# Performance work log

Measured on AMD Instinct MI355X. Metric: run time of the kernel, lower is better.

## Reference

```python
import jax, jax.numpy as jnp
import numpy as np
from jax import lax


def _conv2d(x, w, b, stride):
    # x: [B,C,H,W], w: [O,I,kh,kw], b: [O]
    y = lax.conv_general_dilated(
        x, w, window_strides=(stride, stride), padding='VALID',
        dimension_numbers=('NCHW', 'OIHW', 'NCHW'))
    return y + b[None, :, None, None]


def setup_inputs() -> dict:
    key = jax.random.key(0)
    ks = jax.random.split(key, 4)
    B, C, H, W = 8, 128, 128, 128
    x = jax.random.normal(ks[0], (B, C, H, W), dtype=jnp.float32)
    # conv weights, scaled like torch default init (~1/sqrt(fan_in))
    Wq = jax.random.normal(ks[1], (C, C, 2, 2), dtype=jnp.float32) / np.sqrt(C * 4)
    Wk = jax.random.normal(ks[2], (C, C, 2, 2), dtype=jnp.float32) / np.sqrt(C * 4)
    Wv = jax.random.normal(ks[3], (C, C, 1, 1), dtype=jnp.float32) / np.sqrt(C)
    bq = jnp.zeros((C,), dtype=jnp.float32)
    bk = jnp.zeros((C,), dtype=jnp.float32)
    bv = jnp.zeros((C,), dtype=jnp.float32)
    return {'x': x, 'Wq': Wq, 'bq': bq, 'Wk': Wk, 'bk': bk, 'Wv': Wv, 'bv': bv}


def reference(x, Wq, bq, Wk, bk, Wv, bv):
    B, C, H, W = x.shape
    # query/key: 2x2 stride-2 convs -> [B, C, (H//2)*(W//2)]
    q = _conv2d(x, Wq, bq, 2).reshape(B, C, -1)
    k = _conv2d(x, Wk, bk, 2).reshape(B, C, -1)
    # value: 1x1 conv -> [B, C, H*W]
    v = _conv2d(x, Wv, bv, 1).reshape(B, C, -1)
    # energy: [B, C, C]
    energy = jnp.einsum('bcn,bdn->bcd', q, k)
    # max-subtract trick: softmax over (row_max - energy)
    energy_new = jnp.max(energy, axis=-1, keepdims=True) - energy
    attention = jax.nn.softmax(energy_new, axis=-1)
    out = jnp.einsum('bcd,bdn->bcn', attention, v)
    return out.reshape(B, C, H, W)
```

## Files before the change

### kernel.cpp

```cpp
#include <hip/hip_runtime.h>
#include <math.h>


typedef float f32x4 __attribute__((ext_vector_type(4)));
typedef short s16x8 __attribute__((ext_vector_type(8)));

__device__ __forceinline__ unsigned short f2bf(float f) {
  union { float f; unsigned u; } v; v.f = f;
  unsigned r = v.u + 0x7FFFu + ((v.u >> 16) & 1u);
  return (unsigned short)(r >> 16);
}
__device__ __forceinline__ float bf2f(unsigned short h) {
  union { unsigned u; float f; } v; v.u = ((unsigned)h) << 16;
  return v.f;
}
__device__ __forceinline__ unsigned pack2(unsigned short a, unsigned short b) {
  return (unsigned)a | ((unsigned)b << 16);
}

__global__ __launch_bounds__(256) void k_prep(
    const float* __restrict__ Wq, const float* __restrict__ Wk,
    unsigned short* __restrict__ Wth, unsigned short* __restrict__ Wtl) {
  const int f = (blockIdx.x * 256 + threadIdx.x) * 4;
  const int row = f >> 9;
  const int k   = f & 511;
  const float* src = (row < 128) ? &Wq[row * 512 + k] : &Wk[(row - 128) * 512 + k];
  float4 v = *(const float4*)src;
  unsigned short h0 = f2bf(v.x), h1 = f2bf(v.y), h2 = f2bf(v.z), h3 = f2bf(v.w);
  unsigned short l0 = f2bf(v.x - bf2f(h0)), l1 = f2bf(v.y - bf2f(h1));
  unsigned short l2 = f2bf(v.z - bf2f(h2)), l3 = f2bf(v.w - bf2f(h3));
  const int di = (k >> 5) * 8192 + row * 32 + (k & 31);
  *(ushort4*)&Wth[di] = make_ushort4(h0, h1, h2, h3);
  *(ushort4*)&Wtl[di] = make_ushort4(l0, l1, l2, l3);
}

__global__ __launch_bounds__(256, 2) void k_conv_energy(
    const float* __restrict__ x,
    const unsigned short* __restrict__ Wth, const unsigned short* __restrict__ Wtl,
    const float* __restrict__ bq, const float* __restrict__ bk,
    float* __restrict__ epart) {
  __shared__ unsigned short LDS[32768];
  unsigned short* Th = LDS;
  unsigned short* Tl = LDS + 16384;

  const int t = threadIdx.x;
  const int nt = blockIdx.x, b = blockIdx.y;
  const int w = t >> 6, lane = t & 63;
  const int lrow = lane & 15, lkb = lane >> 4;

  const int pp = t >> 4;
  const int ci_l = pp >> 1, kh = pp & 1;
  const int i16 = t & 15;
  const int klb = ci_l * 4 + kh * 2;
  const float* xb = x + ((size_t)b << 21);
  const float* xrow = xb + (size_t)ci_l * 16384 + (2 * nt + kh) * 128 + 2 * i16;

  f32x4 acc[4][4];
#pragma unroll
  for (int m = 0; m < 4; ++m)
#pragma unroll
    for (int n = 0; n < 4; ++n) acc[m][n] = (f32x4){0.f, 0.f, 0.f, 0.f};

  s16x8 pfh[2][4], pfl[2][4];
  s16x8 bfh[2][4], bfl[2][4];
  float2 pv[2][4];
  const int aoff = (w * 64 + lrow) * 32 + lkb * 8;

#pragma unroll
  for (int m = 0; m < 4; ++m) {
    pfh[0][m] = *(const s16x8*)&Wth[aoff + m * 512];
    pfl[0][m] = *(const s16x8*)&Wtl[aoff + m * 512];
    pfh[1][m] = *(const s16x8*)&Wth[8192 + aoff + m * 512];
    pfl[1][m] = *(const s16x8*)&Wtl[8192 + aoff + m * 512];
  }
#pragma unroll
  for (int g = 0; g < 4; ++g) pv[1][g] = *(const float2*)&xrow[32 * g];
  {
    unsigned short* Nh = LDS;
    unsigned short* Nl = LDS + 2560;
#pragma unroll
    for (int g = 0; g < 4; ++g) {
      const int n = i16 + 16 * g;
      unsigned short hx = f2bf(pv[1][g].x), hy = f2bf(pv[1][g].y);
      *(unsigned*)&Nh[n * 40 + klb] = pack2(hx, hy);
      *(unsigned*)&Nl[n * 40 + klb] = pack2(f2bf(pv[1][g].x - bf2f(hx)),
                                            f2bf(pv[1][g].y - bf2f(hy)));
    }
  }
#pragma unroll
  for (int g = 0; g < 4; ++g)
    pv[1][g] = *(const float2*)&xrow[(size_t)8 * 16384 + 32 * g];
  __syncthreads();
#pragma unroll
  for (int nf = 0; nf < 4; ++nf) {
    const int bidx = (nf * 16 + lrow) * 40 + lkb * 8;
    bfh[0][nf] = *(const s16x8*)&LDS[bidx];
    bfl[0][nf] = *(const s16x8*)&LDS[2560 + bidx];
  }

#pragma unroll
  for (int step = 0; step < 16; ++step) {
    const int cur = step & 1;
    if (step < 15) {
      unsigned short* Nh = LDS + (cur ^ 1) * 5120;
      unsigned short* Nl = Nh + 2560;
#pragma unroll
      for (int g = 0; g < 4; ++g) {
        const int n = i16 + 16 * g;
        unsigned short hx = f2bf(pv[cur ^ 1][g].x), hy = f2bf(pv[cur ^ 1][g].y);
        *(unsigned*)&Nh[n * 40 + klb] = pack2(hx, hy);
        *(unsigned*)&Nl[n * 40 + klb] = pack2(f2bf(pv[cur ^ 1][g].x - bf2f(hx)),
                                              f2bf(pv[cur ^ 1][g].y - bf2f(hy)));
      }
    }
    __syncthreads();
    if (step < 15) {
      const unsigned short* Bh = LDS + (cur ^ 1) * 5120;
      const unsigned short* Bl = Bh + 2560;
#pragma unroll
      for (int nf = 0; nf < 4; ++nf) {
        const int bidx = (nf * 16 + lrow) * 40 + lkb * 8;
        bfh[cur ^ 1][nf] = *(const s16x8*)&Bh[bidx];
        bfl[cur ^ 1][nf] = *(const s16x8*)&Bl[bidx];
      }
    }
    if (step < 14) {
#pragma unroll
      for (int g = 0; g < 4; ++g)
        pv[cur][g] = *(const float2*)&xrow[(size_t)(step + 2) * 8 * 16384 + 32 * g];
    }
#pragma unroll
    for (int m = 0; m < 4; ++m)
#pragma unroll
      for (int n = 0; n < 4; ++n) {
        acc[m][n] = __builtin_amdgcn_mfma_f32_16x16x32_bf16(pfh[cur][m], bfh[cur][n], acc[m][n], 0, 0, 0);
        acc[m][n] = __builtin_amdgcn_mfma_f32_16x16x32_bf16(pfh[cur][m], bfl[cur][n], acc[m][n], 0, 0, 0);
        acc[m][n] = __builtin_amdgcn_mfma_f32_16x16x32_bf16(pfl[cur][m], bfh[cur][n], acc[m][n], 0, 0, 0);
      }
    if (step < 14) {
      const unsigned short* Wh_n = Wth + (step + 2) * 8192;
      const unsigned short* Wl_n = Wtl + (step + 2) * 8192;
#pragma unroll
      for (int m = 0; m < 4; ++m) {
        pfh[cur][m] = *(const s16x8*)&Wh_n[aoff + m * 512];
        pfl[cur][m] = *(const s16x8*)&Wl_n[aoff + m * 512];
      }
    }
  }
  __syncthreads();

  const float* biasp = (w < 2) ? bq : bk;
  const int rb = (w & 1) * 64;
  float biasr[16];
#pragma unroll
  for (int m = 0; m < 4; ++m)
#pragma unroll
    for (int i = 0; i < 4; ++i)
      biasr[m * 4 + i] = biasp[rb + m * 16 + (lane >> 4) * 4 + i];

#pragma unroll
  for (int m = 0; m < 4; ++m) {
    const int r0 = w * 64 + m * 16 + (lane >> 4) * 4;
#pragma unroll
    for (int n = 0; n < 4; ++n) {
      const int c = n * 16 + lrow;
      const int c8 = c >> 3, c7 = c & 7;
#pragma unroll
      for (int i = 0; i < 4; ++i) {
        const int r = r0 + i;
        const float vv = acc[m][n][i] + biasr[m * 4 + i];
        const unsigned short h = f2bf(vv);
        const unsigned short l = f2bf(vv - bf2f(h));
        const int ad = r * 64 + (((c8 ^ (r & 7))) << 3) + c7;
        Th[ad] = h;
        Tl[ad] = l;
      }
    }
  }
  __syncthreads();

  f32x4 e[4][4];
#pragma unroll
  for (int m = 0; m < 4; ++m)
#pragma unroll
    for (int n = 0; n < 4; ++n) e[m][n] = (f32x4){0.f, 0.f, 0.f, 0.f};

  const int mrow0 = (w >> 1) * 64;
  const int nrow0 = 128 + (w & 1) * 64;
#pragma unroll
  for (int ks = 0; ks < 2; ++ks) {
    const int c8 = ks * 4 + lkb;
    s16x8 qh[4], ql[4], kh8[4], kl8[4];
#pragma unroll
    for (int m = 0; m < 4; ++m) {
      const int r = mrow0 + m * 16 + lrow;
      const int ad = r * 64 + ((c8 ^ (r & 7)) << 3);
      qh[m] = *(const s16x8*)&Th[ad];
      ql[m] = *(const s16x8*)&Tl[ad];
    }
#pragma unroll
    for (int n = 0; n < 4; ++n) {
      const int r = nrow0 + n * 16 + lrow;
      const int ad = r * 64 + ((c8 ^ (r & 7)) << 3);
      kh8[n] = *(const s16x8*)&Th[ad];
      kl8[n] = *(const s16x8*)&Tl[ad];
    }
#pragma unroll
    for (int m = 0; m < 4; ++m)
#pragma unroll
      for (int n = 0; n < 4; ++n) {
        e[m][n] = __builtin_amdgcn_mfma_f32_16x16x32_bf16(qh[m], kh8[n], e[m][n], 0, 0, 0);
        e[m][n] = __builtin_amdgcn_mfma_f32_16x16x32_bf16(qh[m], kl8[n], e[m][n], 0, 0, 0);
        e[m][n] = __builtin_amdgcn_mfma_f32_16x16x32_bf16(ql[m], kh8[n], e[m][n], 0, 0, 0);
      }
  }
  float* ep = epart + ((size_t)b * 64 + nt) * 16384;
#pragma unroll
  for (int m = 0; m < 4; ++m) {
    const int qr = (w >> 1) * 64 + m * 16 + (lane >> 4) * 4;
#pragma unroll
    for (int n = 0; n < 4; ++n) {
      const int kr = (w & 1) * 64 + n * 16 + lrow;
#pragma unroll
      for (int i = 0; i < 4; ++i) ep[(size_t)(qr + i) * 128 + kr] = e[m][n][i];
    }
  }
}

__global__ __launch_bounds__(256) void k_softmax_M(
    const float* __restrict__ epart, const float* __restrict__ Wv,
    const float* __restrict__ bv, float* __restrict__ Mbuf,
    float* __restrict__ outbb) {
  __shared__ float As[4][128];
  const int t = threadIdx.x;
  const int wid = t >> 6, lane = t & 63;
  const int b = blockIdx.x >> 5;
  const int c = (blockIdx.x & 31) * 4 + wid;
  const int d0 = lane * 2;

  float2 s = make_float2(0.f, 0.f);
#pragma unroll 4
  for (int p = 0; p < 64; ++p) {
    float2 e = *(const float2*)&epart[((size_t)b * 64 + p) * 16384 + c * 128 + d0];
    s.x += e.x; s.y += e.y;
  }
  float mn = fminf(s.x, s.y);
#pragma unroll
  for (int off = 1; off < 64; off <<= 1) mn = fminf(mn, __shfl_xor(mn, off));
  const float p0 = expf(mn - s.x);
  const float p1 = expf(mn - s.y);
  float tot = p0 + p1;
#pragma unroll
  for (int off = 1; off < 64; off <<= 1) tot += __shfl_xor(tot, off);
  const float inv = 1.f / tot;
  const float a0 = p0 * inv, a1 = p1 * inv;

  const float2 bvv = *(const float2*)&bv[d0];
  float ob = a0 * bvv.x + a1 * bvv.y;
#pragma unroll
  for (int off = 1; off < 64; off <<= 1) ob += __shfl_xor(ob, off);
  if (lane == 0) outbb[b * 128 + c] = ob;

  As[wid][d0] = a0;
  As[wid][d0 + 1] = a1;
  float m0 = 0.f, m1 = 0.f;
#pragma unroll 4
  for (int d = 0; d < 128; ++d) {
    const float a = As[wid][d];
    const float2 wv = *(const float2*)&Wv[d * 128 + d0];
    m0 = fmaf(a, wv.x, m0);
    m1 = fmaf(a, wv.y, m1);
  }
  *(float2*)&Mbuf[(size_t)b * 16384 + c * 128 + d0] = make_float2(m0, m1);
}

__global__ __launch_bounds__(256) void k_out(
    const float* __restrict__ x, const float* __restrict__ Mbuf,
    const float* __restrict__ outbb, float* __restrict__ out) {
  __shared__ unsigned short Ms[128 * 40];
  __shared__ unsigned short Xs[128 * 40];
  const int t = threadIdx.x;
  const int nt = blockIdx.x, b = blockIdx.y;
  const int wid = t >> 6, lane = t & 63;
  const int wr = wid >> 1, wc = wid & 1;
  const int lrow = lane & 15, lkb = lane >> 4;
  const int am = t >> 1, ak0 = (t & 1) * 16;
  const int xkl = (t >> 5) * 4;
  const int xc0 = (t & 31) * 4;

  const float* xb = x + ((size_t)b << 21);
  const float* Mb = Mbuf + (size_t)b * 16384;
  float* ob = out + ((size_t)b << 21);

  f32x4 acc[4][4];
#pragma unroll
  for (int m = 0; m < 4; ++m)
#pragma unroll
    for (int n = 0; n < 4; ++n) acc[m][n] = (f32x4){0.f, 0.f, 0.f, 0.f};

  for (int step = 0; step < 4; ++step) {
    const int kk = step * 32;
    {
      float w[16];
      *(float4*)&w[0]  = *(const float4*)&Mb[am * 128 + kk + ak0];
      *(float4*)&w[4]  = *(const float4*)&Mb[am * 128 + kk + ak0 + 4];
      *(float4*)&w[8]  = *(const float4*)&Mb[am * 128 + kk + ak0 + 8];
      *(float4*)&w[12] = *(const float4*)&Mb[am * 128 + kk + ak0 + 12];
      unsigned short hs[16];
#pragma unroll
      for (int i = 0; i < 16; ++i) hs[i] = f2bf(w[i]);
      *(uint4*)&Ms[am * 40 + ak0]     = *(uint4*)&hs[0];
      *(uint4*)&Ms[am * 40 + ak0 + 8] = *(uint4*)&hs[8];
    }
#pragma unroll
    for (int q = 0; q < 4; ++q) {
      const int kl = xkl + q;
      float4 v = *(const float4*)&xb[(size_t)(kk + kl) * 16384 + nt * 128 + xc0];
      Xs[(xc0 + 0) * 40 + kl] = f2bf(v.x);
      Xs[(xc0 + 1) * 40 + kl] = f2bf(v.y);
      Xs[(xc0 + 2) * 40 + kl] = f2bf(v.z);
      Xs[(xc0 + 3) * 40 + kl] = f2bf(v.w);
    }
    __syncthreads();
    s16x8 af[4], bf[4];
#pragma unroll
    for (int m = 0; m < 4; ++m)
      af[m] = *(const s16x8*)&Ms[(wr * 64 + m * 16 + lrow) * 40 + lkb * 8];
#pragma unroll
    for (int n = 0; n < 4; ++n)
      bf[n] = *(const s16x8*)&Xs[(wc * 64 + n * 16 + lrow) * 40 + lkb * 8];
#pragma unroll
    for (int m = 0; m < 4; ++m)
#pragma unroll
      for (int n = 0; n < 4; ++n)
        acc[m][n] = __builtin_amdgcn_mfma_f32_16x16x32_bf16(af[m], bf[n], acc[m][n], 0, 0, 0);
    __syncthreads();
  }
#pragma unroll
  for (int m = 0; m < 4; ++m) {
    const int r0 = wr * 64 + m * 16 + (lane >> 4) * 4;
#pragma unroll
    for (int n = 0; n < 4; ++n) {
      const int gc = nt * 128 + wc * 64 + n * 16 + (lane & 15);
#pragma unroll
      for (int i = 0; i < 4; ++i) {
        const int row = r0 + i;
        ob[(size_t)row * 16384 + gc] = acc[m][n][i] + outbb[b * 128 + row];
      }
    }
  }
}

extern "C" void kernel_launch(void* const* d_in, const int* in_sizes, int n_in,
                              void* d_out, int out_size, void* d_ws, size_t ws_size,
                              hipStream_t stream) {
  const float* x  = (const float*)d_in[0];
  const float* Wq = (const float*)d_in[1];
  const float* bq = (const float*)d_in[2];
  const float* Wk = (const float*)d_in[3];
  const float* bk = (const float*)d_in[4];
  const float* Wv = (const float*)d_in[5];
  const float* bv = (const float*)d_in[6];
  float* out = (float*)d_out;
  char* ws = (char*)d_ws;

  float* epart = (float*)ws;
  float* Mbuf  = (float*)(ws + 33554432);
  float* outbb = (float*)(ws + 34078720);
  unsigned short* Wth = (unsigned short*)(ws + 34082816);
  unsigned short* Wtl = (unsigned short*)(ws + 34344960);

  hipLaunchKernelGGL(k_prep, dim3(128), dim3(256), 0, stream, Wq, Wk, Wth, Wtl);
  hipLaunchKernelGGL(k_conv_energy, dim3(64, 8), dim3(256), 0, stream,
                     x, Wth, Wtl, bq, bk, epart);
  hipLaunchKernelGGL(k_softmax_M, dim3(256), dim3(256), 0, stream,
                     epart, Wv, bv, Mbuf, outbb);
  hipLaunchKernelGGL(k_out, dim3(128, 8), dim3(256), 0, stream,
                     x, Mbuf, outbb, out);
}
```

Before: 87.04 us.

## Enlarge conv-energy tile to 128 spatial columns with 512-thread blocks

The fused conv+energy kernel now uses 512-thread blocks, each covering two output rows (128 spatial positions) instead of one. Eight waves split the tile as 4x2 over output channels and spatial columns, so weight fragments are reused across twice the spatial width. This halves the number of per-block partial energy matrices written to and summed from the workspace. The main loop is reordered with a single raw barrier per step, the energy stage runs in four k-chunks with a smaller LDS buffer, and f2bf now uses the native __bf16 conversion. In exchange, fewer blocks are launched (256 instead of 512), registers per thread rise, and there are more barriers in the energy stage.

```diff
diff --git a/kernel.cpp b/kernel.cpp
--- a/kernel.cpp
+++ b/kernel.cpp
@@ -6,9 +6,9 @@
 typedef short s16x8 __attribute__((ext_vector_type(8)));
 
 __device__ __forceinline__ unsigned short f2bf(float f) {
-  union { float f; unsigned u; } v; v.f = f;
-  unsigned r = v.u + 0x7FFFu + ((v.u >> 16) & 1u);
-  return (unsigned short)(r >> 16);
+  union { __bf16 b; unsigned short u; } v;
+  v.b = (__bf16)f;
+  return v.u;
 }
 __device__ __forceinline__ float bf2f(unsigned short h) {
   union { unsigned u; float f; } v; v.u = ((unsigned)h) << 16;
@@ -34,26 +34,27 @@
   *(ushort4*)&Wtl[di] = make_ushort4(l0, l1, l2, l3);
 }
 
-__global__ __launch_bounds__(256, 2) void k_conv_energy(
+__global__ __launch_bounds__(512) void k_conv_energy(
     const float* __restrict__ x,
     const unsigned short* __restrict__ Wth, const unsigned short* __restrict__ Wtl,
     const float* __restrict__ bq, const float* __restrict__ bk,
     float* __restrict__ epart) {
-  __shared__ unsigned short LDS[32768];
+  __shared__ unsigned short LDS[20480];
   unsigned short* Th = LDS;
-  unsigned short* Tl = LDS + 16384;
+  unsigned short* Tl = LDS + 8192;
 
   const int t = threadIdx.x;
   const int nt = blockIdx.x, b = blockIdx.y;
   const int w = t >> 6, lane = t & 63;
+  const int wr = w >> 1, wc = w & 1;
   const int lrow = lane & 15, lkb = lane >> 4;
 
-  const int pp = t >> 4;
-  const int ci_l = pp >> 1, kh = pp & 1;
-  const int i16 = t & 15;
+  const int ci_l = t >> 6;
+  const int kh = (t >> 5) & 1;
+  const int i32 = t & 31;
   const int klb = ci_l * 4 + kh * 2;
   const float* xb = x + ((size_t)b << 21);
-  const float* xrow = xb + (size_t)ci_l * 16384 + (2 * nt + kh) * 128 + 2 * i16;
+  const float* xrow = xb + (size_t)ci_l * 16384 + (4 * nt + kh) * 128 + 2 * i32;
 
   f32x4 acc[4][4];
 #pragma unroll
@@ -61,96 +62,83 @@
 #pragma unroll
     for (int n = 0; n < 4; ++n) acc[m][n] = (f32x4){0.f, 0.f, 0.f, 0.f};
 
-  s16x8 pfh[2][4], pfl[2][4];
-  s16x8 bfh[2][4], bfl[2][4];
+  s16x8 pfh[4], pfl[4];
   float2 pv[2][4];
-  const int aoff = (w * 64 + lrow) * 32 + lkb * 8;
+  const int aoff = (wr * 64 + lrow) * 32 + lkb * 8;
+  const int goff[4] = {0, 64, 256, 320};
 
 #pragma unroll
   for (int m = 0; m < 4; ++m) {
-    pfh[0][m] = *(const s16x8*)&Wth[aoff + m * 512];
-    pfl[0][m] = *(const s16x8*)&Wtl[aoff + m * 512];
-    pfh[1][m] = *(const s16x8*)&Wth[8192 + aoff + m * 512];
-    pfl[1][m] = *(const s16x8*)&Wtl[8192 + aoff + m * 512];
-  }
-#pragma unroll
-  for (int g = 0; g < 4; ++g) pv[1][g] = *(const float2*)&xrow[32 * g];
-  {
-    unsigned short* Nh = LDS;
-    unsigned short* Nl = LDS + 2560;
-#pragma unroll
-    for (int g = 0; g < 4; ++g) {
-      const int n = i16 + 16 * g;
-      unsigned short hx = f2bf(pv[1][g].x), hy = f2bf(pv[1][g].y);
-      *(unsigned*)&Nh[n * 40 + klb] = pack2(hx, hy);
-      *(unsigned*)&Nl[n * 40 + klb] = pack2(f2bf(pv[1][g].x - bf2f(hx)),
-                                            f2bf(pv[1][g].y - bf2f(hy)));
-    }
+    pfh[m] = *(const s16x8*)&Wth[aoff + m * 512];
+    pfl[m] = *(const s16x8*)&Wtl[aoff + m * 512];
+  }
+#pragma unroll
+  for (int g = 0; g < 4; ++g) {
+    float2 v = *(const float2*)&xrow[goff[g]];
+    const int col = i32 + 32 * g;
+    unsigned short hx = f2bf(v.x), hy = f2bf(v.y);
+    *(unsigned*)&LDS[col * 40 + klb] = pack2(hx, hy);
+    *(unsigned*)&LDS[5120 + col * 40 + klb] =
+        pack2(f2bf(v.x - bf2f(hx)), f2bf(v.y - bf2f(hy)));
   }
 #pragma unroll
   for (int g = 0; g < 4; ++g)
-    pv[1][g] = *(const float2*)&xrow[(size_t)8 * 16384 + 32 * g];
+    pv[1][g] = *(const float2*)&xrow[(size_t)8 * 16384 + goff[g]];
   __syncthreads();
-#pragma unroll
-  for (int nf = 0; nf < 4; ++nf) {
-    const int bidx = (nf * 16 + lrow) * 40 + lkb * 8;
-    bfh[0][nf] = *(const s16x8*)&LDS[bidx];
-    bfl[0][nf] = *(const s16x8*)&LDS[2560 + bidx];
-  }
 
 #pragma unroll
   for (int step = 0; step < 16; ++step) {
     const int cur = step & 1;
+    const unsigned short* Bh = LDS + cur * 10240;
+    const unsigned short* Bl = Bh + 5120;
+    s16x8 bfh[4], bfl[4];
+#pragma unroll
+    for (int nf = 0; nf < 4; ++nf) {
+      const int bidx = (wc * 64 + nf * 16 + lrow) * 40 + lkb * 8;
+      bfh[nf] = *(const s16x8*)&Bh[bidx];
+      bfl[nf] = *(const s16x8*)&Bl[bidx];
+    }
+#pragma unroll
+    for (int m = 0; m < 4; ++m)
+#pragma unroll
+      for (int n = 0; n < 4; ++n) {
+        acc[m][n] = __builtin_amdgcn_mfma_f32_16x16x32_bf16(pfh[m], bfh[n], acc[m][n], 0, 0, 0);
+        acc[m][n] = __builtin_amdgcn_mfma_f32_16x16x32_bf16(pfh[m], bfl[n], acc[m][n], 0, 0, 0);
+        acc[m][n] = __builtin_amdgcn_mfma_f32_16x16x32_bf16(pfl[m], bfh[n], acc[m][n], 0, 0, 0);
+      }
     if (step < 15) {
-      unsigned short* Nh = LDS + (cur ^ 1) * 5120;
-      unsigned short* Nl = Nh + 2560;
+      const unsigned short* Wh_n = Wth + (step + 1) * 8192;
+      const unsigned short* Wl_n = Wtl + (step + 1) * 8192;
+#pragma unroll
+      for (int m = 0; m < 4; ++m) {
+        pfh[m] = *(const s16x8*)&Wh_n[aoff + m * 512];
+        pfl[m] = *(const s16x8*)&Wl_n[aoff + m * 512];
+      }
+    }
+    if (step < 14) {
+#pragma unroll
+      for (int g = 0; g < 4; ++g)
+        pv[cur][g] = *(const float2*)&xrow[(size_t)(step + 2) * 8 * 16384 + goff[g]];
+    }
+    if (step < 15) {
+      unsigned short* Nh = LDS + (cur ^ 1) * 10240;
+      unsigned short* Nl = Nh + 5120;
 #pragma unroll
       for (int g = 0; g < 4; ++g) {
-        const int n = i16 + 16 * g;
+        const int col = i32 + 32 * g;
         unsigned short hx = f2bf(pv[cur ^ 1][g].x), hy = f2bf(pv[cur ^ 1][g].y);
-        *(unsigned*)&Nh[n * 40 + klb] = pack2(hx, hy);
-        *(unsigned*)&Nl[n * 40 + klb] = pack2(f2bf(pv[cur ^ 1][g].x - bf2f(hx)),
-                                              f2bf(pv[cur ^ 1][g].y - bf2f(hy)));
-      }
-    }
-    __syncthreads();
-    if (step < 15) {
-      const unsigned short* Bh = LDS + (cur ^ 1) * 5120;
-      const unsigned short* Bl = Bh + 2560;
-#pragma unroll
-      for (int nf = 0; nf < 4; ++nf) {
-        const int bidx = (nf * 16 + lrow) * 40 + lkb * 8;
-        bfh[cur ^ 1][nf] = *(const s16x8*)&Bh[bidx];
-        bfl[cur ^ 1][nf] = *(const s16x8*)&Bl[bidx];
-      }
-    }
-    if (step < 14) {
-#pragma unroll
-      for (int g = 0; g < 4; ++g)
-        pv[cur][g] = *(const float2*)&xrow[(size_t)(step + 2) * 8 * 16384 + 32 * g];
-    }
-#pragma unroll
-    for (int m = 0; m < 4; ++m)
-#pragma unroll
-      for (int n = 0; n < 4; ++n) {
-        acc[m][n] = __builtin_amdgcn_mfma_f32_16x16x32_bf16(pfh[cur][m], bfh[cur][n], acc[m][n], 0, 0, 0);
-        acc[m][n] = __builtin_amdgcn_mfma_f32_16x16x32_bf16(pfh[cur][m], bfl[cur][n], acc[m][n], 0, 0, 0);
-        acc[m][n] = __builtin_amdgcn_mfma_f32_16x16x32_bf16(pfl[cur][m], bfh[cur][n], acc[m][n], 0, 0, 0);
-      }
-    if (step < 14) {
-      const unsigned short* Wh_n = Wth + (step + 2) * 8192;
-      const unsigned short* Wl_n = Wtl + (step + 2) * 8192;
-#pragma unroll
-      for (int m = 0; m < 4; ++m) {
-        pfh[cur][m] = *(const s16x8*)&Wh_n[aoff + m * 512];
-        pfl[cur][m] = *(const s16x8*)&Wl_n[aoff + m * 512];
-      }
+        *(unsigned*)&Nh[col * 40 + klb] = pack2(hx, hy);
+        *(unsigned*)&Nl[col * 40 + klb] = pack2(f2bf(pv[cur ^ 1][g].x - bf2f(hx)),
+                                                f2bf(pv[cur ^ 1][g].y - bf2f(hy)));
+      }
+      asm volatile("s_waitcnt lgkmcnt(0)" ::: "memory");
+      __builtin_amdgcn_s_barrier();
     }
   }
   __syncthreads();
 
-  const float* biasp = (w < 2) ? bq : bk;
-  const int rb = (w & 1) * 64;
+  const float* biasp = (wr < 2) ? bq : bk;
+  const int rb = (wr & 1) * 64;
   float biasr[16];
 #pragma unroll
   for (int m = 0; m < 4; ++m)
@@ -158,71 +146,78 @@
     for (int i = 0; i < 4; ++i)
       biasr[m * 4 + i] = biasp[rb + m * 16 + (lane >> 4) * 4 + i];
 
-#pragma unroll
-  for (int m = 0; m < 4; ++m) {
-    const int r0 = w * 64 + m * 16 + (lane >> 4) * 4;
-#pragma unroll
-    for (int n = 0; n < 4; ++n) {
-      const int c = n * 16 + lrow;
-      const int c8 = c >> 3, c7 = c & 7;
-#pragma unroll
-      for (int i = 0; i < 4; ++i) {
-        const int r = r0 + i;
-        const float vv = acc[m][n][i] + biasr[m * 4 + i];
-        const unsigned short h = f2bf(vv);
-        const unsigned short l = f2bf(vv - bf2f(h));
-        const int ad = r * 64 + (((c8 ^ (r & 7))) << 3) + c7;
-        Th[ad] = h;
-        Tl[ad] = l;
-      }
-    }
-  }
-  __syncthreads();
-
-  f32x4 e[4][4];
-#pragma unroll
-  for (int m = 0; m < 4; ++m)
-#pragma unroll
-    for (int n = 0; n < 4; ++n) e[m][n] = (f32x4){0.f, 0.f, 0.f, 0.f};
-
-  const int mrow0 = (w >> 1) * 64;
-  const int nrow0 = 128 + (w & 1) * 64;
-#pragma unroll
-  for (int ks = 0; ks < 2; ++ks) {
-    const int c8 = ks * 4 + lkb;
-    s16x8 qh[4], ql[4], kh8[4], kl8[4];
-#pragma unroll
-    for (int m = 0; m < 4; ++m) {
-      const int r = mrow0 + m * 16 + lrow;
-      const int ad = r * 64 + ((c8 ^ (r & 7)) << 3);
-      qh[m] = *(const s16x8*)&Th[ad];
-      ql[m] = *(const s16x8*)&Tl[ad];
-    }
-#pragma unroll
-    for (int n = 0; n < 4; ++n) {
-      const int r = nrow0 + n * 16 + lrow;
-      const int ad = r * 64 + ((c8 ^ (r & 7)) << 3);
-      kh8[n] = *(const s16x8*)&Th[ad];
-      kl8[n] = *(const s16x8*)&Tl[ad];
-    }
-#pragma unroll
-    for (int m = 0; m < 4; ++m)
-#pragma unroll
-      for (int n = 0; n < 4; ++n) {
-        e[m][n] = __builtin_amdgcn_mfma_f32_16x16x32_bf16(qh[m], kh8[n], e[m][n], 0, 0, 0);
-        e[m][n] = __builtin_amdgcn_mfma_f32_16x16x32_bf16(qh[m], kl8[n], e[m][n], 0, 0, 0);
-        e[m][n] = __builtin_amdgcn_mfma_f32_16x16x32_bf16(ql[m], kh8[n], e[m][n], 0, 0, 0);
-      }
-  }
-  float* ep = epart + ((size_t)b * 64 + nt) * 16384;
-#pragma unroll
-  for (int m = 0; m < 4; ++m) {
-    const int qr = (w >> 1) * 64 + m * 16 + (lane >> 4) * 4;
-#pragma unroll
-    for (int n = 0; n < 4; ++n) {
-      const int kr = (w & 1) * 64 + n * 16 + lrow;
-#pragma unroll
-      for (int i = 0; i < 4; ++i) ep[(size_t)(qr + i) * 128 + kr] = e[m][n][i];
+  f32x4 e[2][4];
+#pragma unroll
+  for (int mm = 0; mm < 2; ++mm)
+#pragma unroll
+    for (int nf = 0; nf < 4; ++nf) e[mm][nf] = (f32x4){0.f, 0.f, 0.f, 0.f};
+
+  const int qg = w >> 1;
+  const int kg = w & 1;
+
+#pragma unroll
+  for (int ks = 0; ks < 4; ++ks) {
+    if (wc == (ks >> 1)) {
+#pragma unroll
+      for (int m = 0; m < 4; ++m) {
+        const int r0 = wr * 64 + m * 16 + (lane >> 4) * 4;
+#pragma unroll
+        for (int nn = 0; nn < 2; ++nn) {
+          const int n = 2 * (ks & 1) + nn;
+          const int cl = nn * 16 + lrow;
+          const int cl8 = cl >> 3, c7 = cl & 7;
+#pragma unroll
+          for (int i = 0; i < 4; ++i) {
+            const int r = r0 + i;
+            const float vv = acc[m][n][i] + biasr[m * 4 + i];
+            const unsigned short h = f2bf(vv);
+            const unsigned short l = f2bf(vv - bf2f(h));
+            const int ad = r * 32 + ((cl8 ^ (r & 3)) << 3) + c7;
+            Th[ad] = h;
+            Tl[ad] = l;
+          }
+        }
+      }
+    }
+    __syncthreads();
+    {
+      s16x8 qh[2], ql[2], kh8[4], kl8[4];
+#pragma unroll
+      for (int mm = 0; mm < 2; ++mm) {
+        const int r = qg * 32 + mm * 16 + lrow;
+        const int ad = r * 32 + ((lkb ^ (r & 3)) << 3);
+        qh[mm] = *(const s16x8*)&Th[ad];
+        ql[mm] = *(const s16x8*)&Tl[ad];
+      }
+#pragma unroll
+      for (int nf = 0; nf < 4; ++nf) {
+        const int r = 128 + kg * 64 + nf * 16 + lrow;
+        const int ad = r * 32 + ((lkb ^ (r & 3)) << 3);
+        kh8[nf] = *(const s16x8*)&Th[ad];
+        kl8[nf] = *(const s16x8*)&Tl[ad];
+      }
+#pragma unroll
+      for (int mm = 0; mm < 2; ++mm)
+#pragma unroll
+        for (int nf = 0; nf < 4; ++nf) {
+          e[mm][nf] = __builtin_amdgcn_mfma_f32_16x16x32_bf16(qh[mm], kh8[nf], e[mm][nf], 0, 0, 0);
+          e[mm][nf] = __builtin_amdgcn_mfma_f32_16x16x32_bf16(qh[mm], kl8[nf], e[mm][nf], 0, 0, 0);
+          e[mm][nf] = __builtin_amdgcn_mfma_f32_16x16x32_bf16(ql[mm], kh8[nf], e[mm][nf], 0, 0, 0);
+        }
+    }
+    if (ks < 3) __syncthreads();
+  }
+
+  float* ep = epart + ((size_t)b * 32 + nt) * 16384;
+#pragma unroll
+  for (int mm = 0; mm < 2; ++mm) {
+    const int qr0 = qg * 32 + mm * 16 + (lane >> 4) * 4;
+#pragma unroll
+    for (int nf = 0; nf < 4; ++nf) {
+      const int kc = kg * 64 + nf * 16 + (lane & 15);
+#pragma unroll
+      for (int i = 0; i < 4; ++i)
+        ep[(size_t)(qr0 + i) * 128 + kc] = e[mm][nf][i];
     }
   }
 }
@@ -240,8 +235,8 @@
 
   float2 s = make_float2(0.f, 0.f);
 #pragma unroll 4
-  for (int p = 0; p < 64; ++p) {
-    float2 e = *(const float2*)&epart[((size_t)b * 64 + p) * 16384 + c * 128 + d0];
+  for (int p = 0; p < 32; ++p) {
+    float2 e = *(const float2*)&epart[((size_t)b * 32 + p) * 16384 + c * 128 + d0];
     s.x += e.x; s.y += e.y;
   }
   float mn = fminf(s.x, s.y);
@@ -365,13 +360,13 @@
   char* ws = (char*)d_ws;
 
   float* epart = (float*)ws;
-  float* Mbuf  = (float*)(ws + 33554432);
-  float* outbb = (float*)(ws + 34078720);
-  unsigned short* Wth = (unsigned short*)(ws + 34082816);
-  unsigned short* Wtl = (unsigned short*)(ws + 34344960);
+  float* Mbuf  = (float*)(ws + 16777216);
+  float* outbb = (float*)(ws + 17301504);
+  unsigned short* Wth = (unsigned short*)(ws + 17305600);
+  unsigned short* Wtl = (unsigned short*)(ws + 17567744);
 
   hipLaunchKernelGGL(k_prep, dim3(128), dim3(256), 0, stream, Wq, Wk, Wth, Wtl);
-  hipLaunchKernelGGL(k_conv_energy, dim3(64, 8), dim3(256), 0, stream,
+  hipLaunchKernelGGL(k_conv_energy, dim3(32, 8), dim3(512), 0, stream,
                      x, Wth, Wtl, bq, bk, epart);
   hipLaunchKernelGGL(k_softmax_M, dim3(256), dim3(256), 0, stream,
                      epart, Wv, bv, Mbuf, outbb);
```

New measurement: 81.66 us. 6.2% less time.
